# Optimization experiments

Hardware: AMD Instinct MI355X
Metric: run time of the kernel (lower is better)

The kernel has to match this reference:

```python
import math
import jax, jax.numpy as jnp
import numpy as np

EPS = 1e-12
NHEAD = 12
HEAD_DIM = 64  # d_model // nhead = 768 // 12


def setup_inputs() -> dict:
    key = jax.random.key(0)
    ks = jax.random.split(key, 8)
    L, D, H = 12, 768, 2048
    B, S = 8, 1024
    std = 0.02
    return {
        "x": jax.random.normal(ks[0], (B, S, D), jnp.float32),
        "wq": jax.random.normal(ks[1], (L, D, D), jnp.float32) * std,
        "wk": jax.random.normal(ks[2], (L, D, D), jnp.float32) * std,
        "wv": jax.random.normal(ks[3], (L, D, D), jnp.float32) * std,
        "wo": jax.random.normal(ks[4], (L, D, D), jnp.float32) * std,
        "w1": jax.random.normal(ks[5], (L, H, D), jnp.float32) * std,
        "w2": jax.random.normal(ks[6], (L, D, H), jnp.float32) * std,
        "attn_norm_w": jnp.ones((L, D), jnp.float32),
        "ffn_norm_w": jnp.ones((L, D), jnp.float32),
    }


def _rmsnorm(x, w):
    # x * rsqrt(mean(x^2) + eps) * w
    return x * jax.lax.rsqrt(jnp.mean(x * x, axis=-1, keepdims=True) + EPS) * w


def _block(x, params):
    wq, wk, wv, wo, w1, w2, anw, fnw = params
    B, S, D = x.shape
    # --- attention (manual matmul-softmax-matmul, fp32 softmax) ---
    xn = _rmsnorm(x, anw)
    q = jnp.einsum('bsd,ed->bse', xn, wq).reshape(B, S, NHEAD, HEAD_DIM)
    k = jnp.einsum('bsd,ed->bse', xn, wk).reshape(B, S, NHEAD, HEAD_DIM)
    v = jnp.einsum('bsd,ed->bse', xn, wv).reshape(B, S, NHEAD, HEAD_DIM)
    scores = jnp.einsum('bqhd,bkhd->bhqk', q, k) / math.sqrt(HEAD_DIM)
    probs = jax.nn.softmax(scores.astype(jnp.float32), axis=-1).astype(x.dtype)
    attn = jnp.einsum('bhqk,bkhd->bqhd', probs, v).reshape(B, S, D)
    h = x + jnp.einsum('bsd,ed->bse', attn, wo)
    # --- FFN: w2(silu(w1(h_norm))) ---
    hn = _rmsnorm(h, fnw)
    ff = jnp.einsum('bsh,dh->bsd', jax.nn.silu(jnp.einsum('bsd,hd->bsh', hn, w1)), w2)
    return h + ff


def reference(x, wq, wk, wv, wo, w1, w2, attn_norm_w, ffn_norm_w):
    def step(carry, p):
        return _block(carry, p), None
    out, _ = jax.lax.scan(step, x, (wq, wk, wv, wo, w1, w2, attn_norm_w, ffn_norm_w))
    return out
```

## Files before the change

### kernel.cpp

```cpp
#include <hip/hip_runtime.h>
#include <stdint.h>

typedef unsigned short u16;
typedef unsigned int u32;
typedef __bf16 bf16x8 __attribute__((ext_vector_type(8)));
typedef __bf16 bf16x4 __attribute__((ext_vector_type(4)));
typedef float f32x4 __attribute__((ext_vector_type(4)));

__device__ __forceinline__ u16 f2bf(float f) {
  u32 u = __builtin_bit_cast(u32, f);
  u32 r = (u + 0x7FFFu + ((u >> 16) & 1u)) >> 16;
  return (u16)r;
}

__global__ __launch_bounds__(256)
void convert_w(const float* __restrict__ wq, const float* __restrict__ wk,
               const float* __restrict__ wv, const float* __restrict__ wo,
               const float* __restrict__ w1, const float* __restrict__ w2,
               u16* __restrict__ out) {
  size_t i = ((size_t)blockIdx.x * 256 + threadIdx.x) * 4;
  if (i >= 5505024) return;
  const float* src; size_t off;
  if (i < 589824)       { src = wq; off = i; }
  else if (i < 1179648) { src = wk; off = i - 589824; }
  else if (i < 1769472) { src = wv; off = i - 1179648; }
  else if (i < 2359296) { src = wo; off = i - 1769472; }
  else if (i < 3932160) { src = w1; off = i - 2359296; }
  else                  { src = w2; off = i - 3932160; }
  float4 v = *(const float4*)(src + off);
  u32 lo = (u32)f2bf(v.x) | ((u32)f2bf(v.y) << 16);
  u32 hi = (u32)f2bf(v.z) | ((u32)f2bf(v.w) << 16);
  *(uint2*)(out + i) = make_uint2(lo, hi);
}

__device__ __forceinline__ void rn_store4(u16* p, float4 v, float4 w, float sc) {
  u32 lo = (u32)f2bf(v.x * sc * w.x) | ((u32)f2bf(v.y * sc * w.y) << 16);
  u32 hi = (u32)f2bf(v.z * sc * w.z) | ((u32)f2bf(v.w * sc * w.w) << 16);
  *(uint2*)p = make_uint2(lo, hi);
}

__global__ __launch_bounds__(256)
void rmsnorm_k(const float* __restrict__ x, const float* __restrict__ w,
               u16* __restrict__ out) {
  const int tok = (blockIdx.x << 2) + (threadIdx.x >> 6);
  const int l = threadIdx.x & 63;
  const float* xr = x + (size_t)tok * 768;
  float4 v0 = *(const float4*)(xr + l * 4);
  float4 v1 = *(const float4*)(xr + 256 + l * 4);
  float4 v2 = *(const float4*)(xr + 512 + l * 4);
  float ss = v0.x*v0.x + v0.y*v0.y + v0.z*v0.z + v0.w*v0.w
           + v1.x*v1.x + v1.y*v1.y + v1.z*v1.z + v1.w*v1.w
           + v2.x*v2.x + v2.y*v2.y + v2.z*v2.z + v2.w*v2.w;
  ss += __shfl_xor(ss, 1);  ss += __shfl_xor(ss, 2);  ss += __shfl_xor(ss, 4);
  ss += __shfl_xor(ss, 8);  ss += __shfl_xor(ss, 16); ss += __shfl_xor(ss, 32);
  float sc = rsqrtf(ss * (1.f / 768.f) + 1e-12f);
  float4 w0 = *(const float4*)(w + l * 4);
  float4 w1v = *(const float4*)(w + 256 + l * 4);
  float4 w2v = *(const float4*)(w + 512 + l * 4);
  u16* o = out + (size_t)tok * 768;
  rn_store4(o + l * 4, v0, w0, sc);
  rn_store4(o + 256 + l * 4, v1, w1v, sc);
  rn_store4(o + 512 + l * 4, v2, w2v, sc);
}

__device__ __forceinline__ int xcd_swz(int bid, int nwg) {
  if (nwg & 7) return bid;
  return (bid & 7) * (nwg >> 3) + (bid >> 3);
}

#define GEMM_CORE(A_, W_, K_, m0_, n0_)                                             \
  for (int kt = 0; kt < (K_); kt += 64) {                                           \
    __syncthreads();                                                                \
    _Pragma("unroll")                                                               \
    for (int ii = 0; ii < 4; ++ii) {                                                \
      int issue = (w << 2) + ii;                                                    \
      int r = (issue << 3) + (l >> 3);                                              \
      int c = (l & 7) ^ (r & 7);                                                    \
      __builtin_amdgcn_global_load_lds((A_) + (size_t)((m0_) + r) * (K_) + kt + c * 8, \
                                       As + issue * 512, 16, 0, 0);                 \
      __builtin_amdgcn_global_load_lds((W_) + (size_t)((n0_) + r) * (K_) + kt + c * 8, \
                                       Ws + issue * 512, 16, 0, 0);                 \
    }                                                                               \
    __syncthreads();                                                                \
    _Pragma("unroll")                                                               \
    for (int kc = 0; kc < 2; ++kc) {                                                \
      int chunk = lg + (kc << 2);                                                   \
      bf16x8 af[4], bfr[4];                                                         \
      _Pragma("unroll")                                                             \
      for (int i = 0; i < 4; ++i) {                                                 \
        int mr = (wm << 6) + (i << 4) + ll;                                         \
        af[i] = *(const bf16x8*)((const char*)As + mr * 128 + ((chunk ^ (mr & 7)) << 4)); \
        int nr = (wn << 6) + (i << 4) + ll;                                         \
        bfr[i] = *(const bf16x8*)((const char*)Ws + nr * 128 + ((chunk ^ (nr & 7)) << 4)); \
      }                                                                             \
      _Pragma("unroll")                                                             \
      for (int i = 0; i < 4; ++i)                                                   \
        _Pragma("unroll")                                                           \
        for (int j = 0; j < 4; ++j)                                                 \
          acc[i][j] = __builtin_amdgcn_mfma_f32_16x16x32_bf16(af[i], bfr[j], acc[i][j], 0, 0, 0); \
    }                                                                               \
  }

template<int EP>
__global__ __launch_bounds__(256, 2)
void gemm_bt(const u16* __restrict__ A, const u16* __restrict__ W,
             void* __restrict__ outp, const float* __restrict__ Res,
             int M, int N, int K) {
  __shared__ __align__(16) u16 As[128 * 64];
  __shared__ __align__(16) u16 Ws[128 * 64];
  const int tid = threadIdx.x;
  const int w = tid >> 6, l = tid & 63;
  const int lg = l >> 4, ll = l & 15;
  const int ntiles = N >> 7;
  const int wg = xcd_swz(blockIdx.x, gridDim.x);
  const int mt = wg / ntiles, nt = wg - mt * ntiles;
  const int m0 = mt << 7, n0 = nt << 7;
  const int wm = w >> 1, wn = w & 1;

  const f32x4 fz = {0.f, 0.f, 0.f, 0.f};
  f32x4 acc[4][4];
#pragma unroll
  for (int i = 0; i < 4; ++i)
#pragma unroll
    for (int j = 0; j < 4; ++j) acc[i][j] = fz;

  GEMM_CORE(A, W, K, m0, n0)

  const int g4 = lg << 2;
#pragma unroll
  for (int i = 0; i < 4; ++i) {
#pragma unroll
    for (int j = 0; j < 4; ++j) {
      int row0 = m0 + (wm << 6) + (i << 4) + g4;
      int col = n0 + (wn << 6) + (j << 4) + ll;
      f32x4 v = acc[i][j];
      if (EP == 0) {
        u16* o = (u16*)outp;
#pragma unroll
        for (int e = 0; e < 4; ++e) o[(size_t)(row0 + e) * N + col] = f2bf(v[e]);
      } else if (EP == 1) {
        float* o = (float*)outp;
#pragma unroll
        for (int e = 0; e < 4; ++e) {
          size_t idx = (size_t)(row0 + e) * N + col;
          o[idx] = Res[idx] + v[e];
        }
      } else {
        u16* o = (u16*)outp;
#pragma unroll
        for (int e = 0; e < 4; ++e) {
          float xx = v[e];
          o[(size_t)(row0 + e) * N + col] = f2bf(xx / (1.f + __expf(-xx)));
        }
      }
    }
  }
}

__global__ __launch_bounds__(256, 4)
void gemm_bt64(const u16* __restrict__ A, const u16* __restrict__ W,
               float* __restrict__ outp, const float* __restrict__ Res,
               int M, int N, int K) {
  __shared__ __align__(16) u16 As[64 * 64];
  __shared__ __align__(16) u16 Ws[128 * 64];
  const int tid = threadIdx.x;
  const int w = tid >> 6, l = tid & 63;
  const int lg = l >> 4, ll = l & 15;
  const int ntiles = N >> 7;
  const int wg = xcd_swz(blockIdx.x, gridDim.x);
  const int mt = wg / ntiles, nt = wg - mt * ntiles;
  const int m0 = mt << 6, n0 = nt << 7;
  const int wm = w >> 1, wn = w & 1;

  const f32x4 fz = {0.f, 0.f, 0.f, 0.f};
  f32x4 acc[2][4];
#pragma unroll
  for (int i = 0; i < 2; ++i)
#pragma unroll
    for (int j = 0; j < 4; ++j) acc[i][j] = fz;

  for (int kt = 0; kt < K; kt += 64) {
    __syncthreads();
#pragma unroll
    for (int ii = 0; ii < 6; ++ii) {
      int issue = w * 6 + ii;
      if (issue < 8) {
        int r = (issue << 3) + (l >> 3);
        int c = (l & 7) ^ (r & 7);
        __builtin_amdgcn_global_load_lds(A + (size_t)(m0 + r) * K + kt + c * 8,
                                         As + issue * 512, 16, 0, 0);
      } else {
        int is2 = issue - 8;
        int r = (is2 << 3) + (l >> 3);
        int c = (l & 7) ^ (r & 7);
        __builtin_amdgcn_global_load_lds(W + (size_t)(n0 + r) * K + kt + c * 8,
                                         Ws + is2 * 512, 16, 0, 0);
      }
    }
    __syncthreads();
#pragma unroll
    for (int kc = 0; kc < 2; ++kc) {
      int chunk = lg + (kc << 2);
      bf16x8 af[2], bfr[4];
#pragma unroll
      for (int i = 0; i < 2; ++i) {
        int mr = (wm << 5) + (i << 4) + ll;
        af[i] = *(const bf16x8*)((const char*)As + mr * 128 + ((chunk ^ (mr & 7)) << 4));
      }
#pragma unroll
      for (int j = 0; j < 4; ++j) {
        int nr = (wn << 6) + (j << 4) + ll;
        bfr[j] = *(const bf16x8*)((const char*)Ws + nr * 128 + ((chunk ^ (nr & 7)) << 4));
      }
#pragma unroll
      for (int i = 0; i < 2; ++i)
#pragma unroll
        for (int j = 0; j < 4; ++j)
          acc[i][j] = __builtin_amdgcn_mfma_f32_16x16x32_bf16(af[i], bfr[j], acc[i][j], 0, 0, 0);
    }
  }

  const int g4 = lg << 2;
#pragma unroll
  for (int i = 0; i < 2; ++i) {
#pragma unroll
    for (int j = 0; j < 4; ++j) {
      int row0 = m0 + (wm << 5) + (i << 4) + g4;
      int col = n0 + (wn << 6) + (j << 4) + ll;
      f32x4 v = acc[i][j];
#pragma unroll
      for (int e = 0; e < 4; ++e) {
        size_t idx = (size_t)(row0 + e) * N + col;
        outp[idx] = Res[idx] + v[e];
      }
    }
  }
}

__global__ __launch_bounds__(256, 2)
void gemm_qkv(const u16* __restrict__ A, const u16* __restrict__ W,
              u16* __restrict__ Qo, u16* __restrict__ Ko, u16* __restrict__ Vo) {
  __shared__ __align__(16) u16 As[128 * 64];
  __shared__ __align__(16) u16 Ws[128 * 64];
  const int tid = threadIdx.x;
  const int w = tid >> 6, l = tid & 63;
  const int lg = l >> 4, ll = l & 15;
  const int wg = xcd_swz(blockIdx.x, 1152);
  const int mt = wg / 18, nt = wg - mt * 18;
  const int m0 = mt << 7, n0 = nt << 7;
  const int wm = w >> 1, wn = w & 1;
  const int K = 768;

  const f32x4 fz = {0.f, 0.f, 0.f, 0.f};
  f32x4 acc[4][4];
#pragma unroll
  for (int i = 0; i < 4; ++i)
#pragma unroll
    for (int j = 0; j < 4; ++j) acc[i][j] = fz;

  GEMM_CORE(A, W, K, m0, n0)

  const int g4 = lg << 2;
#pragma unroll
  for (int i = 0; i < 4; ++i) {
#pragma unroll
    for (int j = 0; j < 4; ++j) {
      int row0 = m0 + (wm << 6) + (i << 4) + g4;
      int col = n0 + (wn << 6) + (j << 4) + ll;
      f32x4 v = acc[i][j];
      if (nt < 12) {
        u16* o = (nt < 6) ? Qo : Ko;
        int c = (nt < 6) ? col : (col - 768);
#pragma unroll
        for (int e = 0; e < 4; ++e) o[(size_t)(row0 + e) * 768 + c] = f2bf(v[e]);
      } else {
        int c = col - 1536;
        int vrow = ((row0 >> 10) * 768) + c;
        u32 lo = (u32)f2bf(v[0]) | ((u32)f2bf(v[1]) << 16);
        u32 hi = (u32)f2bf(v[2]) | ((u32)f2bf(v[3]) << 16);
        *(uint2*)(Vo + ((size_t)vrow << 10) + (row0 & 1023)) = make_uint2(lo, hi);
      }
    }
  }
}

#define AT_SYNC  asm volatile("s_waitcnt lgkmcnt(0)" ::: "memory"); \
                 __builtin_amdgcn_s_barrier();                      \
                 asm volatile("" ::: "memory")
__global__ __launch_bounds__(256, 2)
void attn_kernel(const u16* __restrict__ Q, const u16* __restrict__ Kg,
                 const u16* __restrict__ Vt, u16* __restrict__ Og) {
  __shared__ __align__(16) __bf16 Ks[128 * 64];
  __shared__ __align__(16) __bf16 Vs[64 * 128];

  const int tid = threadIdx.x;
  const int w = tid >> 6, l = tid & 63;
  const int lg = l >> 4, ll = l & 15;
  const int bid = blockIdx.x;
  const int qt = bid / 96;
  const int bh = bid - (bid / 96) * 96;
  const int b = bh / 12, hh = bh - b * 12;
  const float SC = 0.125f * 1.44269504f;

  __bf16* Pw = Ks + (w << 11);

  bf16x8 qf[2];
  const int tq0 = (b << 10) + (qt << 6) + (w << 4);
#pragma unroll
  for (int kc = 0; kc < 2; ++kc)
    qf[kc] = *(const bf16x8*)(Q + (size_t)(tq0 + ll) * 768 + hh * 64 + kc * 32 + lg * 8);

  bf16x8 kp[4], vp[4];
#define ISSUE_KV(t_)                                                                  \
  { _Pragma("unroll")                                                                 \
    for (int ii = 0; ii < 4; ++ii) {                                                  \
      int issue = (w << 2) + ii;                                                      \
      int r = (issue << 3) + (l >> 3);                                                \
      int c = (l & 7) ^ (r & 7);                                                      \
      kp[ii] = *(const bf16x8*)(Kg + (size_t)((b << 10) + ((t_) << 7) + r) * 768 + hh * 64 + c * 8); \
      int rv = (issue << 2) + (l >> 4);                                               \
      int cv = ll ^ (rv & 7);                                                         \
      vp[ii] = *(const bf16x8*)(Vt + (size_t)((bh << 6) + rv) * 1024 + ((t_) << 7) + cv * 8); \
    } }
#define WRITE_KV                                                                      \
  { _Pragma("unroll")                                                                 \
    for (int ii = 0; ii < 4; ++ii) {                                                  \
      int issue = (w << 2) + ii;                                                      \
      *(bf16x8*)((char*)Ks + issue * 1024 + l * 16) = kp[ii];                         \
      *(bf16x8*)((char*)Vs + issue * 1024 + l * 16) = vp[ii];                         \
    } }

  const f32x4 fz = {0.f, 0.f, 0.f, 0.f};
  f32x4 oacc[4];
#pragma unroll
  for (int i = 0; i < 4; ++i) oacc[i] = fz;
  float mrow = -1e30f, lrow = 0.f;

  ISSUE_KV(0);
  WRITE_KV;
  AT_SYNC;

  for (int kt = 0; kt < 8; ++kt) {
    if (kt < 7) ISSUE_KV(kt + 1);

    f32x4 sa[8];
#pragma unroll
    for (int fn = 0; fn < 8; ++fn) sa[fn] = fz;
    __builtin_amdgcn_s_setprio(1);
#pragma unroll
    for (int kc = 0; kc < 2; ++kc) {
      int chunk = lg + (kc << 2);
      bf16x8 kb[8];
#pragma unroll
      for (int fn = 0; fn < 8; ++fn) {
        int nr = (fn << 4) + ll;
        kb[fn] = *(const bf16x8*)((const char*)Ks + nr * 128 + ((chunk ^ (nr & 7)) << 4));
      }
#pragma unroll
      for (int fn = 0; fn < 8; ++fn)
        sa[fn] = __builtin_amdgcn_mfma_f32_16x16x32_bf16(kb[fn], qf[kc], sa[fn], 0, 0, 0);
    }
    __builtin_amdgcn_s_setprio(0);

    AT_SYNC;

    f32x4 vm = sa[0];
#pragma unroll
    for (int fn = 1; fn < 8; ++fn) {
#pragma unroll
      for (int e = 0; e < 4; ++e) vm[e] = fmaxf(vm[e], sa[fn][e]);
    }
    float mx = fmaxf(fmaxf(vm[0], vm[1]), fmaxf(vm[2], vm[3]));
    mx = fmaxf(mx, __shfl_xor(mx, 16));
    mx = fmaxf(mx, __shfl_xor(mx, 32));

    float mnew = mrow, scal = 1.f;
    bool rescale = !__all(mx - mrow <= 8.f);
    if (rescale) {
      mnew = fmaxf(mrow, mx);
      scal = __builtin_amdgcn_exp2f(SC * (mrow - mnew));
#pragma unroll
      for (int fd = 0; fd < 4; ++fd) oacc[fd] *= scal;
      mrow = mnew;
    }
    float c2 = mnew * SC;

    f32x4 vsum = fz;
#pragma unroll
    for (int fn = 0; fn < 8; ++fn) {
      f32x4 p;
#pragma unroll
      for (int e = 0; e < 4; ++e)
        p[e] = __builtin_amdgcn_exp2f(__builtin_fmaf(SC, sa[fn][e], -c2));
      vsum += p;
      bf16x4 pv4;
#pragma unroll
      for (int e = 0; e < 4; ++e) pv4[e] = (__bf16)p[e];
      int chunk = (fn << 1) + (lg >> 1);
      *(bf16x4*)((char*)Pw + ll * 256 + ((chunk ^ (ll & 7)) << 4) + ((lg & 1) << 3)) = pv4;
    }
    float rs = (vsum[0] + vsum[1]) + (vsum[2] + vsum[3]);
    rs += __shfl_xor(rs, 16);
    rs += __shfl_xor(rs, 32);
    lrow = lrow * scal + rs;

    asm volatile("" ::: "memory");

    __builtin_amdgcn_s_setprio(1);
#pragma unroll
    for (int ch = 0; ch < 4; ++ch) {
      int chunk = lg + (ch << 2);
      bf16x8 pb = *(const bf16x8*)((const char*)Pw + ll * 256 + ((chunk ^ (ll & 7)) << 4));
#pragma unroll
      for (int fd = 0; fd < 4; ++fd) {
        int dr = (fd << 4) + ll;
        bf16x8 av = *(const bf16x8*)((const char*)Vs + dr * 256 + ((chunk ^ (dr & 7)) << 4));
        oacc[fd] = __builtin_amdgcn_mfma_f32_16x16x32_bf16(av, pb, oacc[fd], 0, 0, 0);
      }
    }
    __builtin_amdgcn_s_setprio(0);

    if (kt < 7) {
      AT_SYNC;
      WRITE_KV;
      AT_SYNC;
    }
  }
#undef ISSUE_KV
#undef WRITE_KV

  float inv = 1.f / lrow;
#pragma unroll
  for (int fd = 0; fd < 4; ++fd) {
    f32x4 v = oacc[fd];
    int d0 = (fd << 4) + (lg << 2);
    u16* o = Og + (size_t)(tq0 + ll) * 768 + hh * 64 + d0;
    u32 lo = (u32)f2bf(v[0] * inv) | ((u32)f2bf(v[1] * inv) << 16);
    u32 hi = (u32)f2bf(v[2] * inv) | ((u32)f2bf(v[3] * inv) << 16);
    *(uint2*)o = make_uint2(lo, hi);
  }
}

extern "C" void kernel_launch(void* const* d_in, const int* in_sizes, int n_in,
                              void* d_out, int out_size, void* d_ws, size_t ws_size,
                              hipStream_t stream) {
  const float* x = (const float*)d_in[0];
  const float* wq = (const float*)d_in[1];
  const float* wk = (const float*)d_in[2];
  const float* wv = (const float*)d_in[3];
  const float* wo = (const float*)d_in[4];
  const float* w1 = (const float*)d_in[5];
  const float* w2 = (const float*)d_in[6];
  const float* anw = (const float*)d_in[7];
  const float* fnw = (const float*)d_in[8];

  char* ws = (char*)d_ws;
  float* h    = (float*)(ws);
  u16* xn     = (u16*)(ws + 25165824);
  u16* qb     = (u16*)(ws + 37748736);
  u16* kb     = (u16*)(ws + 50331648);
  u16* vt     = (u16*)(ws + 62914560);
  u16* ff1    = (u16*)(ws + 75497472);
  u16* wbuf   = (u16*)(ws + 109051904);

  hipMemcpyAsync(h, x, 25165824, hipMemcpyDeviceToDevice, stream);

  for (int L = 0; L < 12; ++L) {
    convert_w<<<5376, 256, 0, stream>>>(
        wq + (size_t)L * 589824, wk + (size_t)L * 589824,
        wv + (size_t)L * 589824, wo + (size_t)L * 589824,
        w1 + (size_t)L * 1572864, w2 + (size_t)L * 1572864, wbuf);
    rmsnorm_k<<<2048, 256, 0, stream>>>(h, anw + L * 768, xn);
    gemm_qkv<<<1152, 256, 0, stream>>>(xn, wbuf, qb, kb, vt);
    attn_kernel<<<1536, 256, 0, stream>>>(qb, kb, vt, qb);
    gemm_bt64<<<768, 256, 0, stream>>>(qb, wbuf + 1769472, h, h, 8192, 768, 768);
    rmsnorm_k<<<2048, 256, 0, stream>>>(h, fnw + L * 768, xn);
    gemm_bt<2><<<1024, 256, 0, stream>>>(xn, wbuf + 2359296, ff1, nullptr, 8192, 2048, 768);
    float* outw = (L == 11) ? (float*)d_out : h;
    gemm_bt64<<<768, 256, 0, stream>>>(ff1, wbuf + 3932160, outw, h, 8192, 768, 2048);
  }
}
```

Measured before the change: 2.536 ms.

## Load attention K fragments directly into registers and convert all weights upfront

The attention kernel no longer stages K through shared memory. Each wave loads its K MFMA fragments straight from global memory into double-buffered registers, which removes one barrier per tile and the K LDS writes. P now gets its own LDS buffer. Separately, if the workspace is large enough, all 12 layers of weights are converted to bf16 in one launch instead of 12 per-layer launches. The trade-offs are higher register pressure (kb[2][8][2]) that may hurt occupancy at launch_bounds(256,2), uncoalesced K global loads, and a larger workspace requirement.

```diff
diff --git a/kernel.cpp b/kernel.cpp
--- a/kernel.cpp
+++ b/kernel.cpp
@@ -31,6 +31,28 @@
   u32 lo = (u32)f2bf(v.x) | ((u32)f2bf(v.y) << 16);
   u32 hi = (u32)f2bf(v.z) | ((u32)f2bf(v.w) << 16);
   *(uint2*)(out + i) = make_uint2(lo, hi);
+}
+
+__global__ __launch_bounds__(256)
+void convert_w_all(const float* __restrict__ wq, const float* __restrict__ wk,
+                   const float* __restrict__ wv, const float* __restrict__ wo,
+                   const float* __restrict__ w1, const float* __restrict__ w2,
+                   u16* __restrict__ out) {
+  size_t ig = ((size_t)blockIdx.x * 256 + threadIdx.x) * 4;
+  if (ig >= 66060288) return;
+  int L = (int)(ig / 5505024);
+  size_t i = ig - (size_t)L * 5505024;
+  const float* src; size_t off;
+  if (i < 589824)       { src = wq + (size_t)L * 589824;  off = i; }
+  else if (i < 1179648) { src = wk + (size_t)L * 589824;  off = i - 589824; }
+  else if (i < 1769472) { src = wv + (size_t)L * 589824;  off = i - 1179648; }
+  else if (i < 2359296) { src = wo + (size_t)L * 589824;  off = i - 1769472; }
+  else if (i < 3932160) { src = w1 + (size_t)L * 1572864; off = i - 2359296; }
+  else                  { src = w2 + (size_t)L * 1572864; off = i - 3932160; }
+  float4 v = *(const float4*)(src + off);
+  u32 lo = (u32)f2bf(v.x) | ((u32)f2bf(v.y) << 16);
+  u32 hi = (u32)f2bf(v.z) | ((u32)f2bf(v.w) << 16);
+  *(uint2*)(out + ig) = make_uint2(lo, hi);
 }
 
 __device__ __forceinline__ void rn_store4(u16* p, float4 v, float4 w, float sc) {
@@ -290,8 +312,8 @@
 __global__ __launch_bounds__(256, 2)
 void attn_kernel(const u16* __restrict__ Q, const u16* __restrict__ Kg,
                  const u16* __restrict__ Vt, u16* __restrict__ Og) {
-  __shared__ __align__(16) __bf16 Ks[128 * 64];
   __shared__ __align__(16) __bf16 Vs[64 * 128];
+  __shared__ __align__(16) __bf16 Ps[4][16 * 128];
 
   const int tid = threadIdx.x;
   const int w = tid >> 6, l = tid & 63;
@@ -302,7 +324,7 @@
   const int b = bh / 12, hh = bh - b * 12;
   const float SC = 0.125f * 1.44269504f;
 
-  __bf16* Pw = Ks + (w << 11);
+  __bf16* Pw = &Ps[w][0];
 
   bf16x8 qf[2];
   const int tq0 = (b << 10) + (qt << 6) + (w << 4);
@@ -310,23 +332,29 @@
   for (int kc = 0; kc < 2; ++kc)
     qf[kc] = *(const bf16x8*)(Q + (size_t)(tq0 + ll) * 768 + hh * 64 + kc * 32 + lg * 8);
 
-  bf16x8 kp[4], vp[4];
-#define ISSUE_KV(t_)                                                                  \
+  bf16x8 kb[2][8][2];
+#define ISSUE_K(par_, t_)                                                             \
+  { _Pragma("unroll")                                                                 \
+    for (int fn = 0; fn < 8; ++fn)                                                    \
+      _Pragma("unroll")                                                               \
+      for (int kc = 0; kc < 2; ++kc)                                                  \
+        kb[par_][fn][kc] = *(const bf16x8*)(                                          \
+            Kg + (size_t)((b << 10) + ((t_) << 7) + (fn << 4) + ll) * 768             \
+               + hh * 64 + kc * 32 + lg * 8);                                         \
+  }
+
+  bf16x8 vp[4];
+#define ISSUE_V(t_)                                                                   \
+  { _Pragma("unroll")                                                                 \
+    for (int ii = 0; ii < 4; ++ii) {                                                  \
+      int rv = ((w << 2) + ii) * 4 + (l >> 4);                                        \
+      int cv = ll ^ (rv & 7);                                                         \
+      vp[ii] = *(const bf16x8*)(Vt + (size_t)((bh << 6) + rv) * 1024 + ((t_) << 7) + cv * 8); \
+    } }
+#define WRITE_V                                                                       \
   { _Pragma("unroll")                                                                 \
     for (int ii = 0; ii < 4; ++ii) {                                                  \
       int issue = (w << 2) + ii;                                                      \
-      int r = (issue << 3) + (l >> 3);                                                \
-      int c = (l & 7) ^ (r & 7);                                                      \
-      kp[ii] = *(const bf16x8*)(Kg + (size_t)((b << 10) + ((t_) << 7) + r) * 768 + hh * 64 + c * 8); \
-      int rv = (issue << 2) + (l >> 4);                                               \
-      int cv = ll ^ (rv & 7);                                                         \
-      vp[ii] = *(const bf16x8*)(Vt + (size_t)((bh << 6) + rv) * 1024 + ((t_) << 7) + cv * 8); \
-    } }
-#define WRITE_KV                                                                      \
-  { _Pragma("unroll")                                                                 \
-    for (int ii = 0; ii < 4; ++ii) {                                                  \
-      int issue = (w << 2) + ii;                                                      \
-      *(bf16x8*)((char*)Ks + issue * 1024 + l * 16) = kp[ii];                         \
       *(bf16x8*)((char*)Vs + issue * 1024 + l * 16) = vp[ii];                         \
     } }
 
@@ -336,33 +364,26 @@
   for (int i = 0; i < 4; ++i) oacc[i] = fz;
   float mrow = -1e30f, lrow = 0.f;
 
-  ISSUE_KV(0);
-  WRITE_KV;
+  ISSUE_V(0);
+  WRITE_V;
+  ISSUE_K(0, 0);
   AT_SYNC;
 
+#pragma unroll
   for (int kt = 0; kt < 8; ++kt) {
-    if (kt < 7) ISSUE_KV(kt + 1);
+    const int par = kt & 1;
+    if (kt < 7) { ISSUE_V(kt + 1); ISSUE_K(par ^ 1, kt + 1); }
 
     f32x4 sa[8];
 #pragma unroll
     for (int fn = 0; fn < 8; ++fn) sa[fn] = fz;
     __builtin_amdgcn_s_setprio(1);
 #pragma unroll
-    for (int kc = 0; kc < 2; ++kc) {
-      int chunk = lg + (kc << 2);
-      bf16x8 kb[8];
-#pragma unroll
-      for (int fn = 0; fn < 8; ++fn) {
-        int nr = (fn << 4) + ll;
-        kb[fn] = *(const bf16x8*)((const char*)Ks + nr * 128 + ((chunk ^ (nr & 7)) << 4));
-      }
+    for (int kc = 0; kc < 2; ++kc)
 #pragma unroll
       for (int fn = 0; fn < 8; ++fn)
-        sa[fn] = __builtin_amdgcn_mfma_f32_16x16x32_bf16(kb[fn], qf[kc], sa[fn], 0, 0, 0);
-    }
+        sa[fn] = __builtin_amdgcn_mfma_f32_16x16x32_bf16(kb[par][fn][kc], qf[kc], sa[fn], 0, 0, 0);
     __builtin_amdgcn_s_setprio(0);
-
-    AT_SYNC;
 
     f32x4 vm = sa[0];
 #pragma unroll
@@ -374,16 +395,16 @@
     mx = fmaxf(mx, __shfl_xor(mx, 16));
     mx = fmaxf(mx, __shfl_xor(mx, 32));
 
-    float mnew = mrow, scal = 1.f;
+    float scal = 1.f;
     bool rescale = !__all(mx - mrow <= 8.f);
     if (rescale) {
-      mnew = fmaxf(mrow, mx);
+      float mnew = fmaxf(mrow, mx);
       scal = __builtin_amdgcn_exp2f(SC * (mrow - mnew));
 #pragma unroll
       for (int fd = 0; fd < 4; ++fd) oacc[fd] *= scal;
       mrow = mnew;
     }
-    float c2 = mnew * SC;
+    float c2 = mrow * SC;
 
     f32x4 vsum = fz;
 #pragma unroll
@@ -422,12 +443,13 @@
 
     if (kt < 7) {
       AT_SYNC;
-      WRITE_KV;
+      WRITE_V;
       AT_SYNC;
     }
   }
-#undef ISSUE_KV
-#undef WRITE_KV
+#undef ISSUE_K
+#undef ISSUE_V
+#undef WRITE_V
 
   float inv = 1.f / lrow;
 #pragma unroll
@@ -463,20 +485,29 @@
   u16* ff1    = (u16*)(ws + 75497472);
   u16* wbuf   = (u16*)(ws + 109051904);
 
+  const bool upfront = ws_size >= 109051904ull + 132120576ull;
+
   hipMemcpyAsync(h, x, 25165824, hipMemcpyDeviceToDevice, stream);
+  if (upfront)
+    convert_w_all<<<64512, 256, 0, stream>>>(wq, wk, wv, wo, w1, w2, wbuf);
 
   for (int L = 0; L < 12; ++L) {
-    convert_w<<<5376, 256, 0, stream>>>(
-        wq + (size_t)L * 589824, wk + (size_t)L * 589824,
-        wv + (size_t)L * 589824, wo + (size_t)L * 589824,
-        w1 + (size_t)L * 1572864, w2 + (size_t)L * 1572864, wbuf);
+    u16* wL = wbuf;
+    if (upfront) {
+      wL = wbuf + (size_t)L * 5505024;
+    } else {
+      convert_w<<<5376, 256, 0, stream>>>(
+          wq + (size_t)L * 589824, wk + (size_t)L * 589824,
+          wv + (size_t)L * 589824, wo + (size_t)L * 589824,
+          w1 + (size_t)L * 1572864, w2 + (size_t)L * 1572864, wbuf);
+    }
     rmsnorm_k<<<2048, 256, 0, stream>>>(h, anw + L * 768, xn);
-    gemm_qkv<<<1152, 256, 0, stream>>>(xn, wbuf, qb, kb, vt);
+    gemm_qkv<<<1152, 256, 0, stream>>>(xn, wL, qb, kb, vt);
     attn_kernel<<<1536, 256, 0, stream>>>(qb, kb, vt, qb);
-    gemm_bt64<<<768, 256, 0, stream>>>(qb, wbuf + 1769472, h, h, 8192, 768, 768);
+    gemm_bt64<<<768, 256, 0, stream>>>(qb, wL + 1769472, h, h, 8192, 768, 768);
     rmsnorm_k<<<2048, 256, 0, stream>>>(h, fnw + L * 768, xn);
-    gemm_bt<2><<<1024, 256, 0, stream>>>(xn, wbuf + 2359296, ff1, nullptr, 8192, 2048, 768);
+    gemm_bt<2><<<1024, 256, 0, stream>>>(xn, wL + 2359296, ff1, nullptr, 8192, 2048, 768);
     float* outw = (L == 11) ? (float*)d_out : h;
-    gemm_bt64<<<768, 256, 0, stream>>>(ff1, wbuf + 3932160, outw, h, 8192, 768, 2048);
-  }
-}
+    gemm_bt64<<<768, 256, 0, stream>>>(ff1, wL + 3932160, outw, h, 8192, 768, 2048);
+  }
+}
```

Result: slower. 3.149 ms (+24.2%).
